# Kernel tuning notes

Hardware: AMD Instinct MI355X
Metric: run time of the kernel (lower is better)

## Reference

```python
import jax, jax.numpy as jnp
import numpy as np

N_NODES = 100000


def gcn_conv(x, W, b, src, dst, n_nodes):
    """PyG GCNConv: out = D^{-1/2} (A + I) D^{-1/2} X W + b."""
    h = x @ W  # [N, F_out]
    # add self-loops
    loop = jnp.arange(n_nodes, dtype=src.dtype)
    s = jnp.concatenate([src, loop])
    d = jnp.concatenate([dst, loop])
    # symmetric normalization (deg counts incoming edges incl. self-loop)
    deg = jax.ops.segment_sum(jnp.ones_like(d, dtype=h.dtype), d, num_segments=n_nodes)
    dinv = jnp.where(deg > 0, jax.lax.rsqrt(deg), 0.0)
    coef = dinv[s] * dinv[d]  # [E+N]
    msg = h[s] * coef[:, None]  # gather + scale
    out = jax.ops.segment_sum(msg, d, num_segments=n_nodes)  # scatter-add
    return out + b


def setup_inputs() -> dict:
    key = jax.random.key(0)
    k1, k2, k3, k4, k5, k6 = jax.random.split(key, 6)
    in_dim, hidden_dim, out_dim = 128, 64, 64
    n_edges = 1000000
    x = jax.random.normal(k1, (N_NODES, in_dim), dtype=jnp.float32)
    edge_index = jax.random.randint(k2, (2, n_edges), 0, N_NODES, dtype=jnp.int64)
    # glorot-style init for GCN weights
    W1 = jax.random.normal(k3, (in_dim, hidden_dim), dtype=jnp.float32) / np.sqrt(in_dim)
    b1 = jnp.zeros((hidden_dim,), dtype=jnp.float32)
    W2 = jax.random.normal(k4, (hidden_dim, out_dim), dtype=jnp.float32) / np.sqrt(hidden_dim)
    b2 = jnp.zeros((out_dim,), dtype=jnp.float32)
    return {"x": x, "edge_index": edge_index, "W1": W1, "b1": b1, "W2": W2, "b2": b2}


def reference(x, edge_index, W1, b1, W2, b2):
    src, dst = edge_index[0], edge_index[1]
    h = jax.nn.relu(gcn_conv(x, W1, b1, src, dst, N_NODES))
    out = gcn_conv(h, W2, b2, src, dst, N_NODES)
    return out
```

## Files before the change

kernel.cpp:

```cpp
#include <hip/hip_runtime.h>


#define MD 48

typedef __attribute__((ext_vector_type(8))) short bf16x8;
typedef __attribute__((ext_vector_type(4))) float f32x4;
typedef __attribute__((ext_vector_type(4))) int   i32x4;
typedef __attribute__((ext_vector_type(4))) unsigned u32x4;

__device__ inline float bf2f(unsigned short v) {
    unsigned u = (unsigned)v << 16;
    return __builtin_bit_cast(float, u);
}
__device__ inline unsigned short f2bf(float f) {
    unsigned u = __builtin_bit_cast(unsigned, f);
    unsigned r = (u + 0x7FFFu + ((u >> 16) & 1u)) >> 16;
    return (unsigned short)r;
}

__device__ inline void convW_one(const float* __restrict__ W, short* __restrict__ Wth,
                                 short* __restrict__ Wtl, int K, int k, int f) {
    float v = W[k * 64 + f];
    unsigned b = __builtin_bit_cast(unsigned, v);
    unsigned hb = b & 0xFFFF0000u;
    float d = v - __builtin_bit_cast(float, hb);
    unsigned lb = __builtin_bit_cast(unsigned, d);
    Wth[f * K + k] = (short)(hb >> 16);
    Wtl[f * K + k] = (short)(lb >> 16);
}

__global__ __launch_bounds__(256) void k_prep(int* __restrict__ cnt, int n, int nbz,
                                              const float* __restrict__ W1,
                                              short* __restrict__ W1th, short* __restrict__ W1tl,
                                              const float* __restrict__ W2,
                                              short* __restrict__ W2th, short* __restrict__ W2tl) {
    const int b = blockIdx.x;
    if (b < nbz) {
        int i = b * 256 + threadIdx.x;
        if (i < n) cnt[i] = 0;
    } else if (b < nbz + 128) {
        if (threadIdx.x < 64) convW_one(W1, W1th, W1tl, 128, b - nbz, threadIdx.x);
    } else {
        if (threadIdx.x < 64) convW_one(W2, W2th, W2tl, 64, b - nbz - 128, threadIdx.x);
    }
}

__global__ __launch_bounds__(256) void k_fill_xcd(const int* __restrict__ src,
                                                  const int* __restrict__ dst, int E,
                                                  int* __restrict__ cnt,
                                                  int* __restrict__ col_ell, int npx) {
    const int myxcd = blockIdx.x & 7;
    const int lo = myxcd * npx;
    const int hi = lo + npx;
    const int vb = blockIdx.x >> 3;
    const int nvb = gridDim.x >> 3;
    const int tid = vb * 256 + threadIdx.x;
    const int nthr = nvb * 256;
    for (int base = tid * 4; base < E; base += nthr * 4) {
        i32x4 d4 = *(const i32x4*)&dst[base];
#pragma unroll
        for (int k = 0; k < 4; ++k) {
            int d = d4[k];
            if (d >= lo && d < hi) {
                int p = atomicAdd(&cnt[d], 1);
                if (p < MD) col_ell[(size_t)d * MD + p] = src[base + k];
            }
        }
    }
}

template <int K>
__global__ __launch_bounds__(256) void k_mm_f32A(const float* __restrict__ X,
                                                 const short* __restrict__ Wth,
                                                 const short* __restrict__ Wtl,
                                                 const int* __restrict__ cnt,
                                                 unsigned short* __restrict__ G, int n) {
    const int lane = threadIdx.x & 63;
    const int w = threadIdx.x >> 6;
    const int r0 = lane & 15;
    const int kq = lane >> 4;
    const int arow = blockIdx.x * 64 + w * 16 + r0;
    const float* xrow = X + (size_t)(arow < n ? arow : n - 1) * K;

    f32x4 acc[4] = {};
#pragma unroll
    for (int kc = 0; kc < K / 32; ++kc) {
        const int ks = kc * 32 + kq * 8;
        float xv[8];
        *(f32x4*)&xv[0] = __builtin_nontemporal_load((const f32x4*)&xrow[ks]);
        *(f32x4*)&xv[4] = __builtin_nontemporal_load((const f32x4*)&xrow[ks + 4]);
        bf16x8 ah, al;
#pragma unroll
        for (int j = 0; j < 8; ++j) {
            unsigned b = __builtin_bit_cast(unsigned, xv[j]);
            unsigned hb = b & 0xFFFF0000u;
            float d = xv[j] - __builtin_bit_cast(float, hb);
            unsigned lb = __builtin_bit_cast(unsigned, d);
            ah[j] = (short)(hb >> 16);
            al[j] = (short)(lb >> 16);
        }
#pragma unroll
        for (int c = 0; c < 4; ++c) {
            bf16x8 bh = *(const bf16x8*)&Wth[(c * 16 + r0) * K + ks];
            bf16x8 bl = *(const bf16x8*)&Wtl[(c * 16 + r0) * K + ks];
            acc[c] = __builtin_amdgcn_mfma_f32_16x16x32_bf16(ah, bh, acc[c], 0, 0, 0);
            acc[c] = __builtin_amdgcn_mfma_f32_16x16x32_bf16(ah, bl, acc[c], 0, 0, 0);
            acc[c] = __builtin_amdgcn_mfma_f32_16x16x32_bf16(al, bh, acc[c], 0, 0, 0);
        }
    }
    const int orow = blockIdx.x * 64 + w * 16 + kq * 4;
#pragma unroll
    for (int rg = 0; rg < 4; ++rg) {
        int gr = orow + rg;
        if (gr < n) {
            float di = rsqrtf((float)(cnt[gr] + 1));
#pragma unroll
            for (int c = 0; c < 4; ++c)
                G[(size_t)gr * 64 + c * 16 + r0] = f2bf(acc[c][rg] * di);
        }
    }
}

__global__ __launch_bounds__(256) void k_mm_bf16A(const unsigned short* __restrict__ A,
                                                  const short* __restrict__ Wth,
                                                  const short* __restrict__ Wtl,
                                                  const int* __restrict__ cnt,
                                                  unsigned short* __restrict__ G, int n) {
    constexpr int K = 64;
    const int lane = threadIdx.x & 63;
    const int w = threadIdx.x >> 6;
    const int r0 = lane & 15;
    const int kq = lane >> 4;
    const int arow = blockIdx.x * 64 + w * 16 + r0;
    const unsigned short* ar = A + (size_t)(arow < n ? arow : n - 1) * K;

    f32x4 acc[4] = {};
#pragma unroll
    for (int kc = 0; kc < K / 32; ++kc) {
        const int ks = kc * 32 + kq * 8;
        bf16x8 a = __builtin_nontemporal_load((const bf16x8*)&ar[ks]);
#pragma unroll
        for (int c = 0; c < 4; ++c) {
            bf16x8 bh = *(const bf16x8*)&Wth[(c * 16 + r0) * K + ks];
            bf16x8 bl = *(const bf16x8*)&Wtl[(c * 16 + r0) * K + ks];
            acc[c] = __builtin_amdgcn_mfma_f32_16x16x32_bf16(a, bh, acc[c], 0, 0, 0);
            acc[c] = __builtin_amdgcn_mfma_f32_16x16x32_bf16(a, bl, acc[c], 0, 0, 0);
        }
    }
    const int orow = blockIdx.x * 64 + w * 16 + kq * 4;
#pragma unroll
    for (int rg = 0; rg < 4; ++rg) {
        int gr = orow + rg;
        if (gr < n) {
            float di = rsqrtf((float)(cnt[gr] + 1));
#pragma unroll
            for (int c = 0; c < 4; ++c)
                G[(size_t)gr * 64 + c * 16 + r0] = f2bf(acc[c][rg] * di);
        }
    }
}

template <bool RELU, bool OUTBF>
__global__ __launch_bounds__(256) void k_gather8(const unsigned short* __restrict__ g,
                                                 const int* __restrict__ cntArr,
                                                 const int* __restrict__ col_ell,
                                                 const float* __restrict__ bias,
                                                 void* __restrict__ dest, int n) {
    const int node = blockIdx.x * 4 + (threadIdx.x >> 6);
    if (node >= n) return;
    const int lane = threadIdx.x & 63;
    const int grp = lane >> 3;
    const int fl = lane & 7;
    const int cn = cntArr[node];
    const int lc = min(cn, MD);
    const float dn = rsqrtf((float)(cn + 1));
    const int myidx = col_ell[(size_t)node * MD + lane];

    float acc[8] = {};
    if (grp == 0) {
        u32x4 u = *(const u32x4*)&g[(size_t)node * 64 + fl * 8];
#pragma unroll
        for (int k = 0; k < 4; ++k) {
            acc[2 * k]     = bf2f((unsigned short)(u[k] & 0xFFFF));
            acc[2 * k + 1] = bf2f((unsigned short)(u[k] >> 16));
        }
    }
    for (int j8 = 0; j8 < lc; j8 += 8) {
        int j = j8 + grp;
        int s = __shfl(myidx, j);
        if (j < lc) {
            u32x4 u = *(const u32x4*)&g[(size_t)s * 64 + fl * 8];
#pragma unroll
            for (int k = 0; k < 4; ++k) {
                acc[2 * k]     += bf2f((unsigned short)(u[k] & 0xFFFF));
                acc[2 * k + 1] += bf2f((unsigned short)(u[k] >> 16));
            }
        }
    }
#pragma unroll
    for (int k = 0; k < 8; ++k) {
        acc[k] += __shfl_xor(acc[k], 8);
        acc[k] += __shfl_xor(acc[k], 16);
        acc[k] += __shfl_xor(acc[k], 32);
    }
    if (grp == 0) {
        float v[8];
        const float* bv = &bias[fl * 8];
#pragma unroll
        for (int k = 0; k < 8; ++k) {
            v[k] = fmaf(acc[k], dn, bv[k]);
            if (RELU) v[k] = fmaxf(v[k], 0.f);
        }
        if (OUTBF) {
            u32x4 o;
            o[0] = (unsigned)f2bf(v[0]) | ((unsigned)f2bf(v[1]) << 16);
            o[1] = (unsigned)f2bf(v[2]) | ((unsigned)f2bf(v[3]) << 16);
            o[2] = (unsigned)f2bf(v[4]) | ((unsigned)f2bf(v[5]) << 16);
            o[3] = (unsigned)f2bf(v[6]) | ((unsigned)f2bf(v[7]) << 16);
            *(u32x4*)&((unsigned short*)dest)[(size_t)node * 64 + fl * 8] = o;
        } else {
            float* dp = &((float*)dest)[(size_t)node * 64 + fl * 8];
            __builtin_nontemporal_store(*(const f32x4*)&v[0], (f32x4*)&dp[0]);
            __builtin_nontemporal_store(*(const f32x4*)&v[4], (f32x4*)&dp[4]);
        }
    }
}

extern "C" void kernel_launch(void* const* d_in, const int* in_sizes, int n_in,
                              void* d_out, int out_size, void* d_ws, size_t ws_size,
                              hipStream_t stream) {
    const float* x  = (const float*)d_in[0];
    const int*   ei = (const int*)d_in[1];
    const float* W1 = (const float*)d_in[2];
    const float* b1 = (const float*)d_in[3];
    const float* W2 = (const float*)d_in[4];
    const float* b2 = (const float*)d_in[5];

    const int N = in_sizes[0] / 128;
    const int E = in_sizes[1] / 2;
    const int* src = ei;
    const int* dst = ei + E;
    float* out = (float*)d_out;

    char* ws = (char*)d_ws;
    size_t off = 0;
    auto alloc = [&](size_t bytes) {
        void* p = ws + off;
        off += (bytes + 63) & ~(size_t)63;
        return p;
    };
    unsigned short* a1   = (unsigned short*)alloc((size_t)N * 64 * 2);
    unsigned short* gbuf = (unsigned short*)alloc((size_t)N * 64 * 2);
    int*   cnt     = (int*)alloc((size_t)N * 4);
    int*   col_ell = (int*)alloc(((size_t)N * MD + 64) * 4);
    short* W1th    = (short*)alloc((size_t)64 * 128 * 2);
    short* W1tl    = (short*)alloc((size_t)64 * 128 * 2);
    short* W2th    = (short*)alloc((size_t)64 * 64 * 2);
    short* W2tl    = (short*)alloc((size_t)64 * 64 * 2);

    const int NBZ   = (N + 255) / 256;
    const int NB_MM = (N + 63) / 64;
    const int NB_G  = (N + 3) / 4;
    const int npx   = (N + 7) / 8;

    k_prep<<<NBZ + 192, 256, 0, stream>>>(cnt, N, NBZ, W1, W1th, W1tl, W2, W2th, W2tl);

    k_fill_xcd<<<8192, 256, 0, stream>>>(src, dst, E, cnt, col_ell, npx);

    k_mm_f32A<128><<<NB_MM, 256, 0, stream>>>(x, W1th, W1tl, cnt, gbuf, N);
    k_gather8<true, true><<<NB_G, 256, 0, stream>>>(gbuf, cnt, col_ell, b1, a1, N);

    k_mm_bf16A<<<NB_MM, 256, 0, stream>>>(a1, W2th, W2tl, cnt, gbuf, N);
    k_gather8<false, false><<<NB_G, 256, 0, stream>>>(gbuf, cnt, col_ell, b2, out, N);
}
```

Baseline: 187.1 us.

## Transpose ELL column layout to slot-major and pack gather accumulators as float2

Stores the ELL neighbor index table slot-major (p*N + d) rather than node-major. The fill kernel's writes from different nodes in the same slot become closer together, and the gather kernel's per-lane index load now has a stride of N. The gather accumulators are also restructured into float2 vectors so the compiler can emit packed FP32 adds, and the bf16 unpack is simplified. The trade-off is that each wave's index load turns into 48 scattered accesses instead of one contiguous 192-byte read.

Result: slower. 203.2 us (+8.6%).

```diff
diff --git a/kernel.cpp b/kernel.cpp
--- a/kernel.cpp
+++ b/kernel.cpp
@@ -5,6 +5,7 @@
 
 typedef __attribute__((ext_vector_type(8))) short bf16x8;
 typedef __attribute__((ext_vector_type(4))) float f32x4;
+typedef __attribute__((ext_vector_type(2))) float f32x2;
 typedef __attribute__((ext_vector_type(4))) int   i32x4;
 typedef __attribute__((ext_vector_type(4))) unsigned u32x4;
 
@@ -48,7 +49,8 @@
 __global__ __launch_bounds__(256) void k_fill_xcd(const int* __restrict__ src,
                                                   const int* __restrict__ dst, int E,
                                                   int* __restrict__ cnt,
-                                                  int* __restrict__ col_ell, int npx) {
+                                                  int* __restrict__ col_ell,
+                                                  int npx, int N) {
     const int myxcd = blockIdx.x & 7;
     const int lo = myxcd * npx;
     const int hi = lo + npx;
@@ -63,7 +65,7 @@
             int d = d4[k];
             if (d >= lo && d < hi) {
                 int p = atomicAdd(&cnt[d], 1);
-                if (p < MD) col_ell[(size_t)d * MD + p] = src[base + k];
+                if (p < MD) col_ell[(size_t)p * N + d] = src[base + k];
             }
         }
     }
@@ -165,7 +167,7 @@
                                                  const int* __restrict__ cntArr,
                                                  const int* __restrict__ col_ell,
                                                  const float* __restrict__ bias,
-                                                 void* __restrict__ dest, int n) {
+                                                 void* __restrict__ dest, int n, int N) {
     const int node = blockIdx.x * 4 + (threadIdx.x >> 6);
     if (node >= n) return;
     const int lane = threadIdx.x & 63;
@@ -174,15 +176,18 @@
     const int cn = cntArr[node];
     const int lc = min(cn, MD);
     const float dn = rsqrtf((float)(cn + 1));
-    const int myidx = col_ell[(size_t)node * MD + lane];
-
-    float acc[8] = {};
+    const int cl = min(lane, MD - 1);
+    const int myidx = col_ell[(size_t)cl * N + node];
+
+    f32x2 acc2[4] = {};
     if (grp == 0) {
         u32x4 u = *(const u32x4*)&g[(size_t)node * 64 + fl * 8];
 #pragma unroll
         for (int k = 0; k < 4; ++k) {
-            acc[2 * k]     = bf2f((unsigned short)(u[k] & 0xFFFF));
-            acc[2 * k + 1] = bf2f((unsigned short)(u[k] >> 16));
+            f32x2 f;
+            f[0] = __builtin_bit_cast(float, u[k] << 16);
+            f[1] = __builtin_bit_cast(float, u[k] & 0xFFFF0000u);
+            acc2[k] += f;
         }
     }
     for (int j8 = 0; j8 < lc; j8 += 8) {
@@ -192,24 +197,34 @@
             u32x4 u = *(const u32x4*)&g[(size_t)s * 64 + fl * 8];
 #pragma unroll
             for (int k = 0; k < 4; ++k) {
-                acc[2 * k]     += bf2f((unsigned short)(u[k] & 0xFFFF));
-                acc[2 * k + 1] += bf2f((unsigned short)(u[k] >> 16));
+                f32x2 f;
+                f[0] = __builtin_bit_cast(float, u[k] << 16);
+                f[1] = __builtin_bit_cast(float, u[k] & 0xFFFF0000u);
+                acc2[k] += f;
             }
         }
     }
 #pragma unroll
-    for (int k = 0; k < 8; ++k) {
-        acc[k] += __shfl_xor(acc[k], 8);
-        acc[k] += __shfl_xor(acc[k], 16);
-        acc[k] += __shfl_xor(acc[k], 32);
+    for (int m = 8; m <= 32; m <<= 1) {
+#pragma unroll
+        for (int k = 0; k < 4; ++k) {
+            f32x2 o;
+            o[0] = __shfl_xor(acc2[k][0], m);
+            o[1] = __shfl_xor(acc2[k][1], m);
+            acc2[k] += o;
+        }
     }
     if (grp == 0) {
         float v[8];
         const float* bv = &bias[fl * 8];
 #pragma unroll
-        for (int k = 0; k < 8; ++k) {
-            v[k] = fmaf(acc[k], dn, bv[k]);
-            if (RELU) v[k] = fmaxf(v[k], 0.f);
+        for (int k = 0; k < 4; ++k) {
+            v[2 * k]     = fmaf(acc2[k][0], dn, bv[2 * k]);
+            v[2 * k + 1] = fmaf(acc2[k][1], dn, bv[2 * k + 1]);
+            if (RELU) {
+                v[2 * k]     = fmaxf(v[2 * k], 0.f);
+                v[2 * k + 1] = fmaxf(v[2 * k + 1], 0.f);
+            }
         }
         if (OUTBF) {
             u32x4 o;
@@ -252,7 +267,7 @@
     unsigned short* a1   = (unsigned short*)alloc((size_t)N * 64 * 2);
     unsigned short* gbuf = (unsigned short*)alloc((size_t)N * 64 * 2);
     int*   cnt     = (int*)alloc((size_t)N * 4);
-    int*   col_ell = (int*)alloc(((size_t)N * MD + 64) * 4);
+    int*   col_ell = (int*)alloc((size_t)N * MD * 4);
     short* W1th    = (short*)alloc((size_t)64 * 128 * 2);
     short* W1tl    = (short*)alloc((size_t)64 * 128 * 2);
     short* W2th    = (short*)alloc((size_t)64 * 64 * 2);
@@ -265,11 +280,11 @@
 
     k_prep<<<NBZ + 192, 256, 0, stream>>>(cnt, N, NBZ, W1, W1th, W1tl, W2, W2th, W2tl);
 
-    k_fill_xcd<<<8192, 256, 0, stream>>>(src, dst, E, cnt, col_ell, npx);
+    k_fill_xcd<<<8192, 256, 0, stream>>>(src, dst, E, cnt, col_ell, npx, N);
 
     k_mm_f32A<128><<<NB_MM, 256, 0, stream>>>(x, W1th, W1tl, cnt, gbuf, N);
-    k_gather8<true, true><<<NB_G, 256, 0, stream>>>(gbuf, cnt, col_ell, b1, a1, N);
+    k_gather8<true, true><<<NB_G, 256, 0, stream>>>(gbuf, cnt, col_ell, b1, a1, N, N);
 
     k_mm_bf16A<<<NB_MM, 256, 0, stream>>>(a1, W2th, W2tl, cnt, gbuf, N);
-    k_gather8<false, false><<<NB_G, 256, 0, stream>>>(gbuf, cnt, col_ell, b2, out, N);
-}
+    k_gather8<false, false><<<NB_G, 256, 0, stream>>>(gbuf, cnt, col_ell, b2, out, N, N);
+}
```
